# Kernel tuning notes

Hardware: AMD Instinct MI355X
Metric: run time of the kernel (lower is better)

Reference implementation:

```python
import jax, jax.numpy as jnp
import numpy as np

N_EMBD = 256
BLOCK_SIZE = 128
N_HEAD = 8
HEAD_SIZE = 256
B = 256
T = 128


def setup_inputs() -> dict:
    key = jax.random.key(0)
    ks = jax.random.split(key, 9)
    s = 0.02
    return {
        "x": jax.random.normal(ks[0], (B, T, N_EMBD), dtype=jnp.float32),
        # torch Linear weight layout: [out_features, in_features], stacked over heads
        "Wq": jax.random.normal(ks[1], (N_HEAD, HEAD_SIZE, N_EMBD), dtype=jnp.float32) * s,
        "bq": jax.random.normal(ks[2], (N_HEAD, HEAD_SIZE), dtype=jnp.float32) * s,
        "Wk": jax.random.normal(ks[3], (N_HEAD, HEAD_SIZE, N_EMBD), dtype=jnp.float32) * s,
        "bk": jax.random.normal(ks[4], (N_HEAD, HEAD_SIZE), dtype=jnp.float32) * s,
        "Wv": jax.random.normal(ks[5], (N_HEAD, HEAD_SIZE, N_EMBD), dtype=jnp.float32) * s,
        "bv": jax.random.normal(ks[6], (N_HEAD, HEAD_SIZE), dtype=jnp.float32) * s,
        "Wp": jax.random.normal(ks[7], (N_EMBD, N_EMBD), dtype=jnp.float32) * s,
        "bp": jax.random.normal(ks[8], (N_EMBD,), dtype=jnp.float32) * s,
    }


def reference(x, Wq, bq, Wk, bk, Wv, bv, Wp, bp):
    Bb, Tt, C = x.shape
    scale = C ** (-0.5)  # NOTE: original scales by n_embd (input C), not head_size
    # per-head projections: [h, b, t, d]
    q = jnp.einsum("btc,hdc->hbtd", x, Wq) + bq[:, None, None, :]
    k = jnp.einsum("btc,hdc->hbtd", x, Wk) + bk[:, None, None, :]
    v = jnp.einsum("btc,hdc->hbtd", x, Wv) + bv[:, None, None, :]
    att = jnp.einsum("hbtd,hbsd->hbts", q, k) * scale  # [h,b,t,s]
    causal = jnp.tril(jnp.ones((Tt, Tt), dtype=bool))
    att = jnp.where(causal, att, -jnp.inf)
    att = jax.nn.softmax(att, axis=-1)
    out = jnp.einsum("hbts,hbsd->hbtd", att, v)
    # torch.cat along dim=0 (batch concat, as written in the source)
    out = out.reshape(out.shape[0] * Bb, Tt, out.shape[-1])  # [h*b, t, head_size]
    return out @ Wp.T + bp
```

## Files before the change

### kernel.cpp

```cpp
#include <hip/hip_runtime.h>
#include <hip/hip_bf16.h>
#include <stdint.h>


#define TT 128

typedef __attribute__((ext_vector_type(8))) short short8;
typedef __attribute__((ext_vector_type(4))) float f32x4;

#define WS_X    0u
#define WS_M    16777216u
#define WS_WM   17825792u
#define WS_WB   18874368u
#define WS_BB   18939904u
#define WS_CQ   18948096u

#define R_T1   0
#define R_P    65536
#define R_UV   98304
#define R_RED  99328
#define LDS_SIZE 101376

#define LGKM0()  asm volatile("s_waitcnt lgkmcnt(0)" ::: "memory")
#define BAR()    do { asm volatile("" ::: "memory"); __builtin_amdgcn_s_barrier(); asm volatile("" ::: "memory"); } while (0)
#define PRIO1()  __builtin_amdgcn_s_setprio(1)
#define PRIO0()  __builtin_amdgcn_s_setprio(0)

__device__ __forceinline__ unsigned short f2bf(float x) {
    union { float f; unsigned u; } v; v.f = x;
    unsigned r = v.u + 0x7FFFu + ((v.u >> 16) & 1u);
    return (unsigned short)(r >> 16);
}
__device__ __forceinline__ unsigned pk2(float a, float b) {
    return (unsigned)f2bf(a) | ((unsigned)f2bf(b) << 16);
}

__global__ __launch_bounds__(256) void convert_pre(
    const float* __restrict__ x,
    const float* __restrict__ Wq, const float* __restrict__ bq,
    const float* __restrict__ Wk, const float* __restrict__ bk,
    const float* __restrict__ Wv, const float* __restrict__ bv,
    const float* __restrict__ Wp, const float* __restrict__ bp,
    char* __restrict__ ws)
{
    extern __shared__ char clds[];
    const int tid = threadIdx.x;
    const int bid = blockIdx.x;

    if (bid < 256) {
        const float* src = x + (size_t)bid * 32768;
        char* dst = ws + WS_X + (size_t)bid * 65536;
        for (int i = tid; i < 8192; i += 256) {
            float4 v = ((const float4*)src)[i];
            int row = i >> 6, c4 = i & 63;
            uint2 u; u.x = pk2(v.x, v.y); u.y = pk2(v.z, v.w);
            *(uint2*)(clds + row * 512 + ((c4 * 8) ^ ((row & 7) << 4))) = u;
        }
        __syncthreads();
        for (int i = tid; i < 4096; i += 256) {
            int l = i & 63, ks = (i >> 6) & 7, g = i >> 9;
            int r = g * 16 + (l & 15);
            int boff = ks * 64 + (l >> 4) * 16;
            uint4 q = *(const uint4*)(clds + r * 512 + (boff ^ ((r & 7) << 4)));
            ((uint4*)dst)[i] = q;
        }
        return;
    }
    if (bid < 384) {
        int id = bid - 256, h = id >> 4, st = id & 15;
        float* wkL = (float*)clds;
        for (int i = tid; i < 4096; i += 256) {
            int d = i >> 4, cc = i & 15;
            wkL[i] = Wk[(size_t)h * 65536 + d * 256 + st * 16 + cc];
        }
        __syncthreads();
        const int c = tid;
        float acc[16];
        #pragma unroll
        for (int j = 0; j < 16; ++j) acc[j] = 0.f;
        #pragma unroll 4
        for (int d = 0; d < 256; ++d) {
            float a = Wq[(size_t)h * 65536 + d * 256 + c];
            #pragma unroll
            for (int j = 0; j < 16; ++j) acc[j] += a * wkL[d * 16 + j];
        }
        char* base = ws + WS_M + (size_t)h * 131072;
        int ks = c >> 5, lgp = (c >> 3) & 3, jb = c & 7;
        #pragma unroll
        for (int j = 0; j < 16; ++j) {
            int cp = st * 16 + j;
            *(unsigned short*)(base + (((st * 8 + ks)) << 10)
                + ((cp & 15) + 16 * lgp) * 16 + jb * 2) = f2bf(acc[j] * 0.0625f);
        }
        return;
    }
    if (bid < 512) {
        int id = bid - 384, h = id >> 4, st = id & 15;
        float* wpL = (float*)clds;
        for (int i = tid; i < 4096; i += 256) {
            int e = i >> 8, d = i & 255;
            wpL[e * 257 + d] = Wp[(size_t)(st * 16 + e) * 256 + d];
        }
        __syncthreads();
        const int c = tid;
        float acc[16];
        #pragma unroll
        for (int j = 0; j < 16; ++j) acc[j] = 0.f;
        #pragma unroll 4
        for (int d = 0; d < 256; ++d) {
            float wv = Wv[(size_t)h * 65536 + d * 256 + c];
            #pragma unroll
            for (int j = 0; j < 16; ++j) acc[j] += wv * wpL[j * 257 + d];
        }
        char* base = ws + WS_WM + (size_t)h * 131072;
        int ks = c >> 5, lgp = (c >> 3) & 3, jb = c & 7;
        #pragma unroll
        for (int j = 0; j < 16; ++j) {
            *(unsigned short*)(base + (((st * 8 + ks)) << 10)
                + (j + 16 * lgp) * 16 + jb * 2) = f2bf(acc[j]);
        }
        return;
    }
    if (bid < 520) {
        const int h = bid - 512;
        {
            uint4 z = {0u,0u,0u,0u};
            for (int i = tid; i < 512; i += 256)
                ((uint4*)(ws + WS_WB + (size_t)h * 8192))[i] = z;
        }
        float* tK = (float*)clds;
        float* tQ = (float*)(clds + 16384);
        const int c = tid;
        float s1 = 0.f, s2 = 0.f;
        for (int d0 = 0; d0 < 256; d0 += 16) {
            __syncthreads();
            for (int i = tid; i < 1024; i += 256) {
                int row = i >> 6, c4 = i & 63;
                ((float4*)tK)[row * 64 + c4] =
                    ((const float4*)(Wk + (size_t)h * 65536 + (size_t)(d0 + row) * 256))[c4];
                ((float4*)tQ)[row * 64 + c4] =
                    ((const float4*)(Wq + (size_t)h * 65536 + (size_t)(d0 + row) * 256))[c4];
            }
            __syncthreads();
            #pragma unroll
            for (int dd = 0; dd < 16; ++dd) {
                s1 += tK[dd * 256 + c] * bq[h * 256 + d0 + dd];
                s2 += tQ[dd * 256 + c] * bk[h * 256 + d0 + dd];
            }
        }
        int ks = c >> 5, lgp = (c >> 3) & 3, jb = c & 7;
        char* base = ws + WS_WB + (size_t)h * 8192 + ks * 1024;
        *(unsigned short*)(base + (0 + 16 * lgp) * 16 + jb * 2) = f2bf(s2 * 0.0625f);
        *(unsigned short*)(base + (1 + 16 * lgp) * 16 + jb * 2) = f2bf(s1 * 0.0625f);
        float* red = (float*)(clds + 32768);
        red[tid] = bq[h * 256 + tid] * bk[h * 256 + tid];
        __syncthreads();
        if (tid == 0) {
            float cq = 0.f;
            for (int d = 0; d < 256; ++d) cq += red[d];
            *(float*)(ws + WS_CQ + h * 4) = cq * 0.0625f;
        }
        return;
    }
    {
        const int st = bid - 520;
        float* wpT = (float*)clds;
        float* bvL = (float*)(clds + 17408);
        for (int i = tid; i < 1024; i += 256) {
            int row = i >> 6, c4 = i & 63;
            float4 v = ((const float4*)(Wp + (size_t)(st * 16 + row) * 256))[c4];
            float* dstp = wpT + row * 257 + c4 * 4;
            dstp[0] = v.x; dstp[1] = v.y; dstp[2] = v.z; dstp[3] = v.w;
        }
        for (int i = tid; i < 512; i += 256)
            ((float4*)bvL)[i] = ((const float4*)bv)[i];
        __syncthreads();
        const int el = tid >> 4, dg = tid & 15;
        #pragma unroll
        for (int h = 0; h < 8; ++h) {
            float p = 0.f;
            #pragma unroll
            for (int dd = 0; dd < 16; ++dd) {
                int d = dg * 16 + dd;
                p += bvL[h * 256 + d] * wpT[el * 257 + d];
            }
            p += __shfl_xor(p, 1);
            p += __shfl_xor(p, 2);
            p += __shfl_xor(p, 4);
            p += __shfl_xor(p, 8);
            if (dg == 0)
                *(float*)(ws + WS_BB + (size_t)h * 1024 + (st * 16 + el) * 4)
                    = bp[st * 16 + el] + p;
        }
        return;
    }
}

__global__ __launch_bounds__(512, 2) void mha_fused(
    const char* __restrict__ ws, float* __restrict__ out)
{
    extern __shared__ char lds[];
    const int tid = threadIdx.x;
    const int w  = tid >> 6, l = tid & 63;
    const int lg = l >> 4, lr = l & 15;
    const int mq = w & 3, nh = w >> 2;
    const int bid = blockIdx.x;
    const int h = bid >> 8, b = bid & 255;

    const char* Xf  = ws + WS_X  + (size_t)b * 65536;
    const char* Mh  = ws + WS_M  + (size_t)h * 131072;
    const char* WMh = ws + WS_WM + (size_t)h * 131072;
    const char* WBh = ws + WS_WB + (size_t)h * 8192;

    short8 xf[2][8];
    #pragma unroll
    for (int mt = 0; mt < 2; ++mt)
        #pragma unroll
        for (int ks = 0; ks < 8; ++ks)
            xf[mt][ks] = *(const short8*)(Xf + (((mq*2 + mt)*8 + ks) << 10) + l*16);

    {
        f32x4 vacc[2] = {f32x4{0.f,0.f,0.f,0.f}, f32x4{0.f,0.f,0.f,0.f}};
        #pragma unroll
        for (int ks = 0; ks < 8; ++ks) {
            short8 wb = *(const short8*)(WBh + (ks << 10) + l*16);
            vacc[0] = __builtin_amdgcn_mfma_f32_16x16x32_bf16(xf[0][ks], wb, vacc[0], 0, 0, 0);
            vacc[1] = __builtin_amdgcn_mfma_f32_16x16x32_bf16(xf[1][ks], wb, vacc[1], 0, 0, 0);
        }
        if (nh == 0 && lr < 2) {
            #pragma unroll
            for (int mt = 0; mt < 2; ++mt)
                #pragma unroll
                for (int r = 0; r < 4; ++r) {
                    int t = mq*32 + mt*16 + lg*4 + r;
                    *(float*)(lds + R_UV + lr*512 + t*4) = vacc[mt][r];
                }
        }
    }

    #pragma unroll
    for (int p = 0; p < 2; ++p) {
        const int ga = nh*8 + p*4;
        f32x4 acc[2][4];
        #pragma unroll
        for (int i = 0; i < 2; ++i)
            #pragma unroll
            for (int j = 0; j < 4; ++j) acc[i][j] = f32x4{0.f,0.f,0.f,0.f};
        #pragma unroll
        for (int ks = 0; ks < 8; ++ks) {
            short8 nb[4];
            #pragma unroll
            for (int nt = 0; nt < 4; ++nt)
                nb[nt] = *(const short8*)(Mh + (((ga+nt)*8 + ks) << 10) + l*16);
            PRIO1();
            #pragma unroll
            for (int mt = 0; mt < 2; ++mt)
                #pragma unroll
                for (int nt = 0; nt < 4; ++nt)
                    acc[mt][nt] = __builtin_amdgcn_mfma_f32_16x16x32_bf16(xf[mt][ks], nb[nt], acc[mt][nt], 0, 0, 0);
            PRIO0();
        }
        #pragma unroll
        for (int mt = 0; mt < 2; ++mt)
            #pragma unroll
            for (int nt = 0; nt < 4; ++nt)
                #pragma unroll
                for (int r = 0; r < 4; ++r) {
                    int t = mq*32 + mt*16 + lg*4 + r;
                    int cp = (ga+nt)*16 + lr;
                    *(unsigned short*)(lds + R_T1 + t*512 + ((cp*2) ^ ((t&7)<<4)))
                        = f2bf(acc[mt][nt][r]);
                }
    }
    LGKM0(); BAR();

    f32x4 sacc[2][4];
    #pragma unroll
    for (int i = 0; i < 2; ++i)
        #pragma unroll
        for (int j = 0; j < 4; ++j) sacc[i][j] = f32x4{0.f,0.f,0.f,0.f};
    #pragma unroll
    for (int ks = 0; ks < 8; ++ks) {
        short8 ta[2];
        #pragma unroll
        for (int mt = 0; mt < 2; ++mt) {
            int t2 = mq*32 + mt*16 + lr;
            ta[mt] = *(const short8*)(lds + R_T1 + t2*512 + ((ks*64 + lg*16) ^ ((t2&7)<<4)));
        }
        short8 sb[4];
        #pragma unroll
        for (int nt = 0; nt < 4; ++nt)
            sb[nt] = *(const short8*)(Xf + (((nh*4+nt)*8 + ks) << 10) + l*16);
        PRIO1();
        #pragma unroll
        for (int mt = 0; mt < 2; ++mt)
            #pragma unroll
            for (int nt = 0; nt < 4; ++nt)
                sacc[mt][nt] = __builtin_amdgcn_mfma_f32_16x16x32_bf16(ta[mt], sb[nt], sacc[mt][nt], 0, 0, 0);
        PRIO0();
    }
    {
        const float cq = *(const float*)(ws + WS_CQ + h*4);
        float uu[4];
        #pragma unroll
        for (int nt = 0; nt < 4; ++nt)
            uu[nt] = *(const float*)(lds + R_UV + 512 + (nh*64 + nt*16 + lr)*4);
        float* redM = (float*)(lds + R_RED);
        float* redS = redM + 256;
        float rmax[2][4];
        #pragma unroll
        for (int mt = 0; mt < 2; ++mt)
            #pragma unroll
            for (int r = 0; r < 4; ++r) {
                int t = mq*32 + mt*16 + lg*4 + r;
                float vt = *(const float*)(lds + R_UV + t*4) + cq;
                float m = -1e30f;
                #pragma unroll
                for (int nt = 0; nt < 4; ++nt) {
                    int s = nh*64 + nt*16 + lr;
                    float sv = sacc[mt][nt][r] + vt + uu[nt];
                    if (s > t) sv = -1e30f;
                    sacc[mt][nt][r] = sv;
                    m = fmaxf(m, sv);
                }
                m = fmaxf(m, __shfl_xor(m, 1));
                m = fmaxf(m, __shfl_xor(m, 2));
                m = fmaxf(m, __shfl_xor(m, 4));
                m = fmaxf(m, __shfl_xor(m, 8));
                rmax[mt][r] = m;
            }
        if (lr == 0) {
            #pragma unroll
            for (int mt = 0; mt < 2; ++mt)
                #pragma unroll
                for (int r = 0; r < 4; ++r)
                    redM[nh*128 + mq*32 + mt*16 + lg*4 + r] = rmax[mt][r];
        }
        LGKM0(); BAR();
        float rsum[2][4];
        #pragma unroll
        for (int mt = 0; mt < 2; ++mt)
            #pragma unroll
            for (int r = 0; r < 4; ++r) {
                int t = mq*32 + mt*16 + lg*4 + r;
                float m = fmaxf(redM[t], redM[128 + t]);
                float ssum = 0.f;
                #pragma unroll
                for (int nt = 0; nt < 4; ++nt) {
                    float p = __expf(sacc[mt][nt][r] - m);
                    sacc[mt][nt][r] = p;
                    ssum += p;
                }
                ssum += __shfl_xor(ssum, 1);
                ssum += __shfl_xor(ssum, 2);
                ssum += __shfl_xor(ssum, 4);
                ssum += __shfl_xor(ssum, 8);
                rsum[mt][r] = ssum;
            }
        if (lr == 0) {
            #pragma unroll
            for (int mt = 0; mt < 2; ++mt)
                #pragma unroll
                for (int r = 0; r < 4; ++r)
                    redS[nh*128 + mq*32 + mt*16 + lg*4 + r] = rsum[mt][r];
        }
        LGKM0(); BAR();
        #pragma unroll
        for (int mt = 0; mt < 2; ++mt)
            #pragma unroll
            for (int r = 0; r < 4; ++r) {
                int t = mq*32 + mt*16 + lg*4 + r;
                float inv = 1.0f / (redS[t] + redS[128 + t]);
                #pragma unroll
                for (int nt = 0; nt < 4; ++nt) {
                    int s = nh*64 + nt*16 + lr;
                    *(unsigned short*)(lds + R_P + t*256 + ((s*2) ^ ((t&7)<<4)))
                        = f2bf(sacc[mt][nt][r] * inv);
                }
            }
    }
    LGKM0(); BAR();

    #pragma unroll
    for (int p = 0; p < 2; ++p) {
        f32x4 acc[2][4];
        #pragma unroll
        for (int i = 0; i < 2; ++i)
            #pragma unroll
            for (int j = 0; j < 4; ++j) acc[i][j] = f32x4{0.f,0.f,0.f,0.f};
        #pragma unroll
        for (int ks = 0; ks < 8; ++ks) {
            short8 wa[2];
            #pragma unroll
            for (int me = 0; me < 2; ++me)
                wa[me] = *(const short8*)(WMh + (((w*2+me)*8 + ks) << 10) + l*16);
            short8 sb[4];
            #pragma unroll
            for (int nt = 0; nt < 4; ++nt)
                sb[nt] = *(const short8*)(Xf + (((p*4+nt)*8 + ks) << 10) + l*16);
            PRIO1();
            #pragma unroll
            for (int me = 0; me < 2; ++me)
                #pragma unroll
                for (int nt = 0; nt < 4; ++nt)
                    acc[me][nt] = __builtin_amdgcn_mfma_f32_16x16x32_bf16(wa[me], sb[nt], acc[me][nt], 0, 0, 0);
            PRIO0();
        }
        #pragma unroll
        for (int me = 0; me < 2; ++me)
            #pragma unroll
            for (int nt = 0; nt < 4; ++nt)
                #pragma unroll
                for (int r = 0; r < 4; ++r) {
                    int e = (w*2+me)*16 + lg*4 + r;
                    int s = (p*4+nt)*16 + lr;
                    *(unsigned short*)(lds + R_T1 + e*256 + ((s*2) ^ ((e&7)<<4)))
                        = f2bf(acc[me][nt][r]);
                }
    }
    LGKM0(); BAR();

    const float* bbp = (const float*)(ws + WS_BB + h*1024);
    short8 pa[2][4];
    #pragma unroll
    for (int mt = 0; mt < 2; ++mt) {
        int t2 = mq*32 + mt*16 + lr;
        #pragma unroll
        for (int ks = 0; ks < 4; ++ks)
            pa[mt][ks] = *(const short8*)(lds + R_P + t2*256 + ((ks*64 + lg*16) ^ ((t2&7)<<4)));
    }
    #pragma unroll
    for (int ec = 0; ec < 4; ++ec) {
        f32x4 acc[2][2];
        #pragma unroll
        for (int i = 0; i < 2; ++i)
            #pragma unroll
            for (int j = 0; j < 2; ++j) acc[i][j] = f32x4{0.f,0.f,0.f,0.f};
        #pragma unroll
        for (int ks = 0; ks < 4; ++ks) {
            short8 hb[2];
            #pragma unroll
            for (int nt = 0; nt < 2; ++nt) {
                int er = (nh*8 + ec*2 + nt)*16 + lr;
                hb[nt] = *(const short8*)(lds + R_T1 + er*256 + ((ks*64 + lg*16) ^ ((er&7)<<4)));
            }
            PRIO1();
            #pragma unroll
            for (int mt = 0; mt < 2; ++mt)
                #pragma unroll
                for (int nt = 0; nt < 2; ++nt)
                    acc[mt][nt] = __builtin_amdgcn_mfma_f32_16x16x32_bf16(pa[mt][ks], hb[nt], acc[mt][nt], 0, 0, 0);
            PRIO0();
        }
        #pragma unroll
        for (int nt = 0; nt < 2; ++nt) {
            int e = (nh*8 + ec*2 + nt)*16 + lr;
            float bbv = bbp[e];
            #pragma unroll
            for (int mt = 0; mt < 2; ++mt)
                #pragma unroll
                for (int r = 0; r < 4; ++r) {
                    int t = mq*32 + mt*16 + lg*4 + r;
                    out[((size_t)bid * TT + t) * 256 + e] = acc[mt][nt][r] + bbv;
                }
        }
    }
}

extern "C" void kernel_launch(void* const* d_in, const int* in_sizes, int n_in,
                              void* d_out, int out_size, void* d_ws, size_t ws_size,
                              hipStream_t stream) {
    (void)in_sizes; (void)n_in; (void)out_size; (void)ws_size;
    const float* x  = (const float*)d_in[0];
    const float* Wq = (const float*)d_in[1];
    const float* bq = (const float*)d_in[2];
    const float* Wk = (const float*)d_in[3];
    const float* bk = (const float*)d_in[4];
    const float* Wv = (const float*)d_in[5];
    const float* bv = (const float*)d_in[6];
    const float* Wp = (const float*)d_in[7];
    const float* bp = (const float*)d_in[8];
    char* ws = (char*)d_ws;

    hipFuncSetAttribute((const void*)convert_pre,
                        hipFuncAttributeMaxDynamicSharedMemorySize, 65536);
    convert_pre<<<dim3(536), dim3(256), 65536, stream>>>(
        x, Wq, bq, Wk, bk, Wv, bv, Wp, bp, ws);

    hipFuncSetAttribute((const void*)mha_fused,
                        hipFuncAttributeMaxDynamicSharedMemorySize, LDS_SIZE);
    mha_fused<<<dim3(2048), dim3(512), LDS_SIZE, stream>>>(ws, (float*)d_out);
}
```

Baseline: 281.9 us.

## Split fused attention stages into halves to shrink LDS and double occupancy

Stages 1 and 4 of the fused kernel are each restructured into two 128-column halves that reuse a 32KB LDS buffer, with extra barriers between halves. This cuts the LDS footprint from about 99KB to 67KB so that launch bounds can request 4 blocks per CU instead of 2. The point is to hide memory and barrier latency with more resident waves. The cost is extra barriers, and register pressure under the tighter launch bound may cause spills.

```diff
diff --git a/kernel.cpp b/kernel.cpp
--- a/kernel.cpp
+++ b/kernel.cpp
@@ -15,11 +15,11 @@
 #define WS_BB   18939904u
 #define WS_CQ   18948096u
 
-#define R_T1   0
-#define R_P    65536
-#define R_UV   98304
-#define R_RED  99328
-#define LDS_SIZE 101376
+#define R_A    0
+#define R_B    32768
+#define R_UV   65536
+#define R_RED  66560
+#define LDS_SIZE 68608
 
 #define LGKM0()  asm volatile("s_waitcnt lgkmcnt(0)" ::: "memory")
 #define BAR()    do { asm volatile("" ::: "memory"); __builtin_amdgcn_s_barrier(); asm volatile("" ::: "memory"); } while (0)
@@ -196,7 +196,7 @@
     }
 }
 
-__global__ __launch_bounds__(512, 2) void mha_fused(
+__global__ __launch_bounds__(512, 4) void mha_fused(
     const char* __restrict__ ws, float* __restrict__ out)
 {
     extern __shared__ char lds[];
@@ -238,9 +238,15 @@
         }
     }
 
+    f32x4 sacc[2][4];
     #pragma unroll
-    for (int p = 0; p < 2; ++p) {
-        const int ga = nh*8 + p*4;
+    for (int i = 0; i < 2; ++i)
+        #pragma unroll
+        for (int j = 0; j < 4; ++j) sacc[i][j] = f32x4{0.f,0.f,0.f,0.f};
+
+    #pragma unroll
+    for (int h2 = 0; h2 < 2; ++h2) {
+        const int ga = h2*8 + nh*4;
         f32x4 acc[2][4];
         #pragma unroll
         for (int i = 0; i < 2; ++i)
@@ -267,38 +273,34 @@
                 #pragma unroll
                 for (int r = 0; r < 4; ++r) {
                     int t = mq*32 + mt*16 + lg*4 + r;
-                    int cp = (ga+nt)*16 + lr;
-                    *(unsigned short*)(lds + R_T1 + t*512 + ((cp*2) ^ ((t&7)<<4)))
+                    int cpl = (nh*4+nt)*16 + lr;
+                    *(unsigned short*)(lds + R_A + t*256 + ((cpl*2) ^ ((t&7)<<4)))
                         = f2bf(acc[mt][nt][r]);
                 }
-    }
-    LGKM0(); BAR();
-
-    f32x4 sacc[2][4];
-    #pragma unroll
-    for (int i = 0; i < 2; ++i)
-        #pragma unroll
-        for (int j = 0; j < 4; ++j) sacc[i][j] = f32x4{0.f,0.f,0.f,0.f};
-    #pragma unroll
-    for (int ks = 0; ks < 8; ++ks) {
-        short8 ta[2];
-        #pragma unroll
-        for (int mt = 0; mt < 2; ++mt) {
-            int t2 = mq*32 + mt*16 + lr;
-            ta[mt] = *(const short8*)(lds + R_T1 + t2*512 + ((ks*64 + lg*16) ^ ((t2&7)<<4)));
-        }
-        short8 sb[4];
-        #pragma unroll
-        for (int nt = 0; nt < 4; ++nt)
-            sb[nt] = *(const short8*)(Xf + (((nh*4+nt)*8 + ks) << 10) + l*16);
-        PRIO1();
-        #pragma unroll
-        for (int mt = 0; mt < 2; ++mt)
+        LGKM0(); BAR();
+        #pragma unroll
+        for (int ks2 = 0; ks2 < 4; ++ks2) {
+            short8 ta[2];
+            #pragma unroll
+            for (int mt = 0; mt < 2; ++mt) {
+                int t2 = mq*32 + mt*16 + lr;
+                ta[mt] = *(const short8*)(lds + R_A + t2*256 + ((ks2*64 + lg*16) ^ ((t2&7)<<4)));
+            }
+            short8 sb[4];
             #pragma unroll
             for (int nt = 0; nt < 4; ++nt)
-                sacc[mt][nt] = __builtin_amdgcn_mfma_f32_16x16x32_bf16(ta[mt], sb[nt], sacc[mt][nt], 0, 0, 0);
-        PRIO0();
-    }
+                sb[nt] = *(const short8*)(Xf + (((nh*4+nt)*8 + (h2*4+ks2)) << 10) + l*16);
+            PRIO1();
+            #pragma unroll
+            for (int mt = 0; mt < 2; ++mt)
+                #pragma unroll
+                for (int nt = 0; nt < 4; ++nt)
+                    sacc[mt][nt] = __builtin_amdgcn_mfma_f32_16x16x32_bf16(ta[mt], sb[nt], sacc[mt][nt], 0, 0, 0);
+            PRIO0();
+        }
+        if (h2 == 0) { LGKM0(); BAR(); }
+    }
+
     {
         const float cq = *(const float*)(ws + WS_CQ + h*4);
         float uu[4];
@@ -374,96 +376,99 @@
                 #pragma unroll
                 for (int nt = 0; nt < 4; ++nt) {
                     int s = nh*64 + nt*16 + lr;
-                    *(unsigned short*)(lds + R_P + t*256 + ((s*2) ^ ((t&7)<<4)))
+                    *(unsigned short*)(lds + R_A + t*256 + ((s*2) ^ ((t&7)<<4)))
                         = f2bf(sacc[mt][nt][r] * inv);
                 }
             }
     }
     LGKM0(); BAR();
 
-    #pragma unroll
-    for (int p = 0; p < 2; ++p) {
-        f32x4 acc[2][4];
-        #pragma unroll
-        for (int i = 0; i < 2; ++i)
-            #pragma unroll
-            for (int j = 0; j < 4; ++j) acc[i][j] = f32x4{0.f,0.f,0.f,0.f};
-        #pragma unroll
-        for (int ks = 0; ks < 8; ++ks) {
-            short8 wa[2];
-            #pragma unroll
-            for (int me = 0; me < 2; ++me)
-                wa[me] = *(const short8*)(WMh + (((w*2+me)*8 + ks) << 10) + l*16);
-            short8 sb[4];
-            #pragma unroll
-            for (int nt = 0; nt < 4; ++nt)
-                sb[nt] = *(const short8*)(Xf + (((p*4+nt)*8 + ks) << 10) + l*16);
-            PRIO1();
-            #pragma unroll
-            for (int me = 0; me < 2; ++me)
-                #pragma unroll
-                for (int nt = 0; nt < 4; ++nt)
-                    acc[me][nt] = __builtin_amdgcn_mfma_f32_16x16x32_bf16(wa[me], sb[nt], acc[me][nt], 0, 0, 0);
-            PRIO0();
-        }
-        #pragma unroll
-        for (int me = 0; me < 2; ++me)
-            #pragma unroll
-            for (int nt = 0; nt < 4; ++nt)
-                #pragma unroll
-                for (int r = 0; r < 4; ++r) {
-                    int e = (w*2+me)*16 + lg*4 + r;
-                    int s = (p*4+nt)*16 + lr;
-                    *(unsigned short*)(lds + R_T1 + e*256 + ((s*2) ^ ((e&7)<<4)))
-                        = f2bf(acc[me][nt][r]);
-                }
-    }
-    LGKM0(); BAR();
-
-    const float* bbp = (const float*)(ws + WS_BB + h*1024);
     short8 pa[2][4];
     #pragma unroll
     for (int mt = 0; mt < 2; ++mt) {
         int t2 = mq*32 + mt*16 + lr;
         #pragma unroll
         for (int ks = 0; ks < 4; ++ks)
-            pa[mt][ks] = *(const short8*)(lds + R_P + t2*256 + ((ks*64 + lg*16) ^ ((t2&7)<<4)));
-    }
+            pa[mt][ks] = *(const short8*)(lds + R_A + t2*256 + ((ks*64 + lg*16) ^ ((t2&7)<<4)));
+    }
+
+    const float* bbp = (const float*)(ws + WS_BB + h*1024);
     #pragma unroll
-    for (int ec = 0; ec < 4; ++ec) {
-        f32x4 acc[2][2];
-        #pragma unroll
-        for (int i = 0; i < 2; ++i)
-            #pragma unroll
-            for (int j = 0; j < 2; ++j) acc[i][j] = f32x4{0.f,0.f,0.f,0.f};
-        #pragma unroll
-        for (int ks = 0; ks < 4; ++ks) {
-            short8 hb[2];
+    for (int eh = 0; eh < 2; ++eh) {
+        {
+            f32x4 acc[2][4];
+            #pragma unroll
+            for (int i = 0; i < 2; ++i)
+                #pragma unroll
+                for (int j = 0; j < 4; ++j) acc[i][j] = f32x4{0.f,0.f,0.f,0.f};
+            #pragma unroll
+            for (int ks = 0; ks < 8; ++ks) {
+                short8 wa[2];
+                #pragma unroll
+                for (int me = 0; me < 2; ++me)
+                    wa[me] = *(const short8*)(WMh + (((eh*8 + mq*2+me)*8 + ks) << 10) + l*16);
+                short8 sb[4];
+                #pragma unroll
+                for (int nt = 0; nt < 4; ++nt)
+                    sb[nt] = *(const short8*)(Xf + (((nh*4 + nt)*8 + ks) << 10) + l*16);
+                PRIO1();
+                #pragma unroll
+                for (int me = 0; me < 2; ++me)
+                    #pragma unroll
+                    for (int nt = 0; nt < 4; ++nt)
+                        acc[me][nt] = __builtin_amdgcn_mfma_f32_16x16x32_bf16(wa[me], sb[nt], acc[me][nt], 0, 0, 0);
+                PRIO0();
+            }
+            #pragma unroll
+            for (int me = 0; me < 2; ++me)
+                #pragma unroll
+                for (int nt = 0; nt < 4; ++nt)
+                    #pragma unroll
+                    for (int r = 0; r < 4; ++r) {
+                        int el = (mq*2+me)*16 + lg*4 + r;
+                        int s  = (nh*4 + nt)*16 + lr;
+                        *(unsigned short*)(lds + R_B + el*256 + ((s*2) ^ ((el&7)<<4)))
+                            = f2bf(acc[me][nt][r]);
+                    }
+        }
+        LGKM0(); BAR();
+        #pragma unroll
+        for (int ec = 0; ec < 2; ++ec) {
+            f32x4 acc[2][2];
+            #pragma unroll
+            for (int i = 0; i < 2; ++i)
+                #pragma unroll
+                for (int j = 0; j < 2; ++j) acc[i][j] = f32x4{0.f,0.f,0.f,0.f};
+            #pragma unroll
+            for (int ks = 0; ks < 4; ++ks) {
+                short8 hb[2];
+                #pragma unroll
+                for (int nt = 0; nt < 2; ++nt) {
+                    int erl = (nh*4 + ec*2 + nt)*16 + lr;
+                    hb[nt] = *(const short8*)(lds + R_B + erl*256 + ((ks*64 + lg*16) ^ ((erl&7)<<4)));
+                }
+                PRIO1();
+                #pragma unroll
+                for (int mt = 0; mt < 2; ++mt)
+                    #pragma unroll
+                    for (int nt = 0; nt < 2; ++nt)
+                        acc[mt][nt] = __builtin_amdgcn_mfma_f32_16x16x32_bf16(pa[mt][ks], hb[nt], acc[mt][nt], 0, 0, 0);
+                PRIO0();
+            }
             #pragma unroll
             for (int nt = 0; nt < 2; ++nt) {
-                int er = (nh*8 + ec*2 + nt)*16 + lr;
-                hb[nt] = *(const short8*)(lds + R_T1 + er*256 + ((ks*64 + lg*16) ^ ((er&7)<<4)));
-            }
-            PRIO1();
-            #pragma unroll
-            for (int mt = 0; mt < 2; ++mt)
-                #pragma unroll
-                for (int nt = 0; nt < 2; ++nt)
-                    acc[mt][nt] = __builtin_amdgcn_mfma_f32_16x16x32_bf16(pa[mt][ks], hb[nt], acc[mt][nt], 0, 0, 0);
-            PRIO0();
-        }
-        #pragma unroll
-        for (int nt = 0; nt < 2; ++nt) {
-            int e = (nh*8 + ec*2 + nt)*16 + lr;
-            float bbv = bbp[e];
-            #pragma unroll
-            for (int mt = 0; mt < 2; ++mt)
-                #pragma unroll
-                for (int r = 0; r < 4; ++r) {
-                    int t = mq*32 + mt*16 + lg*4 + r;
-                    out[((size_t)bid * TT + t) * 256 + e] = acc[mt][nt][r] + bbv;
-                }
-        }
+                int e = eh*128 + (nh*4 + ec*2 + nt)*16 + lr;
+                float bbv = bbp[e];
+                #pragma unroll
+                for (int mt = 0; mt < 2; ++mt)
+                    #pragma unroll
+                    for (int r = 0; r < 4; ++r) {
+                        int t = mq*32 + mt*16 + lg*4 + r;
+                        out[((size_t)bid * TT + t) * 256 + e] = acc[mt][nt][r] + bbv;
+                    }
+            }
+        }
+        if (eh == 0) { LGKM0(); BAR(); }
     }
 }
 
```

Result: slower. 674.6 us (+139.3%).
